# Optimization experiments

Measured on AMD Instinct MI355X. Metric: run time of the kernel, lower is better.

Reference implementation:

```python
import jax, jax.numpy as jnp
import numpy as np


def setup_inputs() -> dict:
    key = jax.random.key(0)
    n_class, n_support, n_query, feature_dim = 32, 16, 16, 1024
    n_rows = n_class * n_support + n_query * n_class  # 1024
    data = jax.random.normal(key, (n_rows, feature_dim), dtype=jnp.float32)
    return {"data": data, "n_class": n_class, "n_support": n_support, "n_query": n_query}


def reference(data, n_class, n_support, n_query):
    D = data.shape[-1]
    # support: [n_class, n_support, D]; query: [n_query*n_class, D]
    support = data[: n_class * n_support].reshape(n_class, n_support, D)
    query = data[n_class * n_support :]
    # attention score: tanh(elementwise product) summed over feature dim
    # scores: [Q, n_class, n_support]  (Q = n_query*n_class)
    scores = jnp.tanh(support[None, :, :, :] * query[:, None, None, :]).sum(-1)
    att = jax.nn.softmax(scores, axis=-1)  # softmax over n_support
    # weighted instance pooling -> prototypes per (query, class): [Q, n_class, D]
    proto = jnp.einsum("qcs,csd->qcd", att, support)
    return proto
```

## Files before the change

### kernel.cpp

```cpp
#include <hip/hip_runtime.h>
#include <stdint.h>

constexpr int NC = 32, NS = 16, NQ = 512, D = 1024;
constexpr int QPB = 8;

typedef float v2f __attribute__((ext_vector_type(2)));
typedef float v4f __attribute__((ext_vector_type(4)));

__device__ __forceinline__ v2f quad_term(v2f t01, v2f t23) {
    v2f A, B;
    A.x = __builtin_amdgcn_exp2f(t01.x);
    A.y = __builtin_amdgcn_exp2f(t01.y);
    B.x = __builtin_amdgcn_exp2f(t23.x);
    B.y = __builtin_amdgcn_exp2f(t23.y);
    A += 1.f;
    B += 1.f;
    v2f prod = A * B;
    v2f sum  = A + B;
    v2f r;
    r.x = __builtin_amdgcn_rcpf(prod.x);
    r.y = __builtin_amdgcn_rcpf(prod.y);
    return sum * r;
}

__device__ __forceinline__ void gload_lds16(const float* g, float* l) {
    __builtin_amdgcn_global_load_lds(
        (const __attribute__((address_space(1))) void*)g,
        (__attribute__((address_space(3))) void*)l,
        16, 0, 0);
}

__global__ __launch_bounds__(256, 2)
void proto_attn_kernel(const float* __restrict__ data, float* __restrict__ out) {
    const int c    = blockIdx.x;
    const int qt   = blockIdx.y;
    const int tid  = threadIdx.x;
    const int wave = tid >> 6;
    const int lane = tid & 63;

    __shared__ __align__(16) float buf[2][NS * 256];

    const float* sup = data + (size_t)c * NS * D;

    auto stage = [&](int p, int b) {
        #pragma unroll
        for (int r = 0; r < 4; ++r) {
            int row = 4 * wave + r;
            gload_lds16(sup + row * D + p * 256 + lane * 4,
                        &buf[b][row * 256]);
        }
    };

    const float K = 2.88539008177792681472f;
    const int q0 = qt * QPB + wave * 2;
    const v4f* qg0 = reinterpret_cast<const v4f*>(data + (size_t)(NC * NS + q0) * D);
    const v4f* qg1 = qg0 + 256;

    stage(0, 0);

    v4f qa[4], qb[4];
    #pragma unroll
    for (int j = 0; j < 4; ++j) {
        qa[j] = qg0[64 * j + lane] * K;
        qb[j] = qg1[64 * j + lane] * K;
    }
    __syncthreads();

    float sc0[NS], sc1[NS];
    #pragma unroll
    for (int s = 0; s < NS; ++s) { sc0[s] = 0.f; sc1[s] = 0.f; }

    #pragma unroll
    for (int p = 0; p < 4; ++p) {
        stage((p + 1) & 3, (p + 1) & 1);
        const v4f* B = reinterpret_cast<const v4f*>(buf[p & 1]);
        const v4f qA = qa[p], qB = qb[p];
        #pragma unroll
        for (int s = 0; s < NS; ++s) {
            v4f sv = B[(s << 6) + lane];
            v2f t0 = quad_term(sv.xy * qA.xy, sv.zw * qA.zw);
            v2f t1 = quad_term(sv.xy * qB.xy, sv.zw * qB.zw);
            sc0[s] += t0.x + t0.y;
            sc1[s] += t1.x + t1.y;
        }
        __syncthreads();
    }

    stage(1, 1);

    #pragma unroll
    for (int s = 0; s < NS; ++s) {
        float r0 = sc0[s], r1 = sc1[s];
        #pragma unroll
        for (int m = 32; m >= 1; m >>= 1) {
            r0 += __shfl_xor(r0, m, 64);
            r1 += __shfl_xor(r1, m, 64);
        }
        sc0[s] = (float)D - 2.f * r0;
        sc1[s] = (float)D - 2.f * r1;
    }

    const float L2E = 1.44269504088896340736f;
    float m0 = sc0[0], m1 = sc1[0];
    #pragma unroll
    for (int s = 1; s < NS; ++s) { m0 = fmaxf(m0, sc0[s]); m1 = fmaxf(m1, sc1[s]); }
    float sum0 = 0.f, sum1 = 0.f;
    #pragma unroll
    for (int s = 0; s < NS; ++s) {
        sc0[s] = __builtin_amdgcn_exp2f((sc0[s] - m0) * L2E);
        sc1[s] = __builtin_amdgcn_exp2f((sc1[s] - m1) * L2E);
        sum0 += sc0[s];
        sum1 += sc1[s];
    }
    const float inv0 = __builtin_amdgcn_rcpf(sum0);
    const float inv1 = __builtin_amdgcn_rcpf(sum1);
    #pragma unroll
    for (int s = 0; s < NS; ++s) { sc0[s] *= inv0; sc1[s] *= inv1; }

    v4f* og0 = reinterpret_cast<v4f*>(out + ((size_t)q0 * NC + c) * D);
    v4f* og1 = reinterpret_cast<v4f*>(out + ((size_t)(q0 + 1) * NC + c) * D);

    #pragma unroll
    for (int p = 0; p < 4; ++p) {
        if (p == 1 || p == 2) stage(p + 1, (p + 1) & 1);
        const v4f* B = reinterpret_cast<const v4f*>(buf[p & 1]);
        v2f oxy0 = 0.f, ozw0 = 0.f, oxy1 = 0.f, ozw1 = 0.f;
        #pragma unroll
        for (int s = 0; s < NS; ++s) {
            v4f sv = B[(s << 6) + lane];
            oxy0 += sv.xy * sc0[s];
            ozw0 += sv.zw * sc0[s];
            oxy1 += sv.xy * sc1[s];
            ozw1 += sv.zw * sc1[s];
        }
        v4f r0, r1;
        r0.xy = oxy0; r0.zw = ozw0;
        r1.xy = oxy1; r1.zw = ozw1;
        og0[(p << 6) + lane] = r0;
        og1[(p << 6) + lane] = r1;
        if (p < 3) __syncthreads();
    }
}

extern "C" void kernel_launch(void* const* d_in, const int* in_sizes, int n_in,
                              void* d_out, int out_size, void* d_ws, size_t ws_size,
                              hipStream_t stream) {
    (void)in_sizes; (void)n_in; (void)out_size; (void)d_ws; (void)ws_size;
    const float* data = (const float*)d_in[0];
    float* out = (float*)d_out;
    dim3 grid(NC, NQ / QPB);
    proto_attn_kernel<<<grid, dim3(256), 0, stream>>>(data, out);
}
```

Measured before the change: 135.7 us.

## Keep the full support tile resident in LDS and reuse it for pooling

```diff
diff --git a/kernel.cpp b/kernel.cpp
--- a/kernel.cpp
+++ b/kernel.cpp
@@ -7,7 +7,7 @@
 typedef float v2f __attribute__((ext_vector_type(2)));
 typedef float v4f __attribute__((ext_vector_type(4)));
 
-__device__ __forceinline__ v2f quad_term(v2f t01, v2f t23) {
+__device__ __forceinline__ void quad_acc(v2f t01, v2f t23, float& acc) {
     v2f A, B;
     A.x = __builtin_amdgcn_exp2f(t01.x);
     A.y = __builtin_amdgcn_exp2f(t01.y);
@@ -17,10 +17,8 @@
     B += 1.f;
     v2f prod = A * B;
     v2f sum  = A + B;
-    v2f r;
-    r.x = __builtin_amdgcn_rcpf(prod.x);
-    r.y = __builtin_amdgcn_rcpf(prod.y);
-    return sum * r;
+    acc = fmaf(sum.x, __builtin_amdgcn_rcpf(prod.x), acc);
+    acc = fmaf(sum.y, __builtin_amdgcn_rcpf(prod.y), acc);
 }
 
 __device__ __forceinline__ void gload_lds16(const float* g, float* l) {
@@ -38,16 +36,17 @@
     const int wave = tid >> 6;
     const int lane = tid & 63;
 
-    __shared__ __align__(16) float buf[2][NS * 256];
+    __shared__ __align__(16) float buf[2][NS * 512];
 
     const float* sup = data + (size_t)c * NS * D;
 
-    auto stage = [&](int p, int b) {
+    auto stage = [&](int h) {
         #pragma unroll
         for (int r = 0; r < 4; ++r) {
             int row = 4 * wave + r;
-            gload_lds16(sup + row * D + p * 256 + lane * 4,
-                        &buf[b][row * 256]);
+            const float* g = sup + row * D + h * 512 + lane * 4;
+            gload_lds16(g,       &buf[h][row * 512]);
+            gload_lds16(g + 256, &buf[h][row * 512 + 256]);
         }
     };
 
@@ -56,7 +55,7 @@
     const v4f* qg0 = reinterpret_cast<const v4f*>(data + (size_t)(NC * NS + q0) * D);
     const v4f* qg1 = qg0 + 256;
 
-    stage(0, 0);
+    stage(0);
 
     v4f qa[4], qb[4];
     #pragma unroll
@@ -70,23 +69,34 @@
     #pragma unroll
     for (int s = 0; s < NS; ++s) { sc0[s] = 0.f; sc1[s] = 0.f; }
 
-    #pragma unroll
-    for (int p = 0; p < 4; ++p) {
-        stage((p + 1) & 3, (p + 1) & 1);
-        const v4f* B = reinterpret_cast<const v4f*>(buf[p & 1]);
-        const v4f qA = qa[p], qB = qb[p];
+    stage(1);
+
+    {
+        const v4f* B = reinterpret_cast<const v4f*>(buf[0]);
         #pragma unroll
         for (int s = 0; s < NS; ++s) {
-            v4f sv = B[(s << 6) + lane];
-            v2f t0 = quad_term(sv.xy * qA.xy, sv.zw * qA.zw);
-            v2f t1 = quad_term(sv.xy * qB.xy, sv.zw * qB.zw);
-            sc0[s] += t0.x + t0.y;
-            sc1[s] += t1.x + t1.y;
+            #pragma unroll
+            for (int j = 0; j < 2; ++j) {
+                v4f sv = B[(s << 7) + (j << 6) + lane];
+                quad_acc(sv.xy * qa[j].xy, sv.zw * qa[j].zw, sc0[s]);
+                quad_acc(sv.xy * qb[j].xy, sv.zw * qb[j].zw, sc1[s]);
+            }
         }
-        __syncthreads();
     }
+    __syncthreads();
 
-    stage(1, 1);
+    {
+        const v4f* B = reinterpret_cast<const v4f*>(buf[1]);
+        #pragma unroll
+        for (int s = 0; s < NS; ++s) {
+            #pragma unroll
+            for (int j = 0; j < 2; ++j) {
+                v4f sv = B[(s << 7) + (j << 6) + lane];
+                quad_acc(sv.xy * qa[2 + j].xy, sv.zw * qa[2 + j].zw, sc0[s]);
+                quad_acc(sv.xy * qb[2 + j].xy, sv.zw * qb[2 + j].zw, sc1[s]);
+            }
+        }
+    }
 
     #pragma unroll
     for (int s = 0; s < NS; ++s) {
@@ -122,12 +132,12 @@
 
     #pragma unroll
     for (int p = 0; p < 4; ++p) {
-        if (p == 1 || p == 2) stage(p + 1, (p + 1) & 1);
-        const v4f* B = reinterpret_cast<const v4f*>(buf[p & 1]);
+        const v4f* B = reinterpret_cast<const v4f*>(buf[p >> 1]);
+        const int jo = (p & 1) << 6;
         v2f oxy0 = 0.f, ozw0 = 0.f, oxy1 = 0.f, ozw1 = 0.f;
         #pragma unroll
         for (int s = 0; s < NS; ++s) {
-            v4f sv = B[(s << 6) + lane];
+            v4f sv = B[(s << 7) + jo + lane];
             oxy0 += sv.xy * sc0[s];
             ozw0 += sv.zw * sc0[s];
             oxy1 += sv.xy * sc1[s];
@@ -138,7 +148,6 @@
         r1.xy = oxy1; r1.zw = ozw1;
         og0[(p << 6) + lane] = r0;
         og1[(p << 6) + lane] = r1;
-        if (p < 3) __syncthreads();
     }
 }
 
```

New measurement: 133.7 us. About the same (-1.5%).
